# Kernel tuning notes

Hardware: AMD Instinct MI355X
Metric: run time of the kernel (lower is better)

## Reference

```python
import jax, jax.numpy as jnp
import numpy as np

B, S, D, H = 2, 2048, 1024, 16
DK = D // H


def setup_inputs() -> dict:
    key = jax.random.key(0)
    ks = jax.random.split(key, 14)
    inp = {
        'query': jax.random.normal(ks[0], (B, S, D), jnp.float32),
        'key': jax.random.normal(ks[1], (B, S, D), jnp.float32),
        'value': jax.random.normal(ks[2], (B, S, D), jnp.float32),
        'mask': jax.random.randint(ks[3], (B, 1, S, S), 0, 2).astype(bool),
        'rel_pos_bias': jax.random.normal(ks[4], (1, H, S, S), jnp.float32),
    }
    scale = 1.0 / np.sqrt(D)
    names = ['Wq', 'bq', 'Wk', 'bk', 'Wv', 'bv', 'Wo', 'bo']
    for i, n in enumerate(names):
        k = ks[5 + i]
        if n.startswith('W'):
            inp[n] = jax.random.normal(k, (D, D), jnp.float32) * scale
        else:
            inp[n] = jnp.zeros((D,), jnp.float32)
    return inp


def reference(query, key, value, mask, rel_pos_bias, Wq, bq, Wk, bk, Wv, bv, Wo, bo):
    # torch Linear: y = x @ W^T + b; W stored [out, in]
    def proj(x, W, b):
        y = x @ W.T + b                       # [B,S,D]
        return y.reshape(B, S, H, DK).transpose(0, 2, 1, 3)  # [B,H,S,DK]

    q = proj(query, Wq, bq)
    k = proj(key, Wk, bk)
    v = proj(value, Wv, bv)

    scores = jnp.einsum('bhqd,bhkd->bhqk', q, k) / jnp.sqrt(jnp.float32(DK))
    scores = scores + rel_pos_bias
    scores = jnp.where(mask, jnp.float32(-1e9), scores)
    p_attn = jax.nn.softmax(scores, axis=-1)
    x = jnp.einsum('bhqk,bhkd->bhqd', p_attn, v)  # [B,H,S,DK]
    x = x.transpose(0, 2, 1, 3).reshape(B, S, D)
    return x @ Wo.T + bo
```

## Files before the change

### kernel.cpp

```cpp
#include <hip/hip_runtime.h>
#include <stdint.h>


typedef _Float16 f16;
typedef _Float16 f16x8 __attribute__((ext_vector_type(8)));
typedef _Float16 f16x4 __attribute__((ext_vector_type(4)));
typedef float f32x4 __attribute__((ext_vector_type(4)));

#define LOG2E 1.44269504088896340736f

__device__ __forceinline__ void gload16(const void* g, void* l) {
  __builtin_amdgcn_global_load_lds(
      (const __attribute__((address_space(1))) unsigned int*)g,
      (__attribute__((address_space(3))) unsigned int*)l, 16, 0, 0);
}

struct CvtSrcs { const float* s[7]; };

__global__ __launch_bounds__(256) void cvt_all(CvtSrcs a, f16* __restrict__ out) {
  const int i = blockIdx.x * 256 + threadIdx.x;
  int r, base;
  if (i < 3145728) { r = i >> 20; base = r << 20; }
  else { r = 3 + ((i - 3145728) >> 18); base = 3145728 + ((r - 3) << 18); }
  const float4 v = ((const float4*)a.s[r])[i - base];
  f16x4 o = {(f16)v.x, (f16)v.y, (f16)v.z, (f16)v.w};
  ((f16x4*)out)[i] = o;
}

__global__ void mask_detect(const uint8_t* __restrict__ m, int* __restrict__ flag) {
  __shared__ int s_off, s_weird;
  const int t = threadIdx.x;
  if (t == 0) { s_off = 0; s_weird = 0; }
  __syncthreads();
  int f_off = 0, f_weird = 0;
  for (int i = t; i < 8192; i += 256) {
    const uint8_t v = m[i];
    if ((i & 3) && v) f_off = 1;
    if (v > 1) f_weird = 1;
  }
  if (f_off) atomicOr(&s_off, 1);
  if (f_weird) atomicOr(&s_weird, 1);
  __syncthreads();
  if (t == 0) *flag = (s_off && !s_weird) ? 1 : 0;
}

__global__ __launch_bounds__(256) void mask_canon(const uint8_t* __restrict__ m,
                                                  uint8_t* __restrict__ out,
                                                  const int* __restrict__ flag) {
  const int i = (blockIdx.x * 256 + threadIdx.x) * 4;
  uchar4 o;
  if (*flag) {
    const uchar4 v = *(const uchar4*)(m + i);
    o = make_uchar4(v.x != 0, v.y != 0, v.z != 0, v.w != 0);
  } else {
    const int4 v = *(const int4*)((const int*)m + i);
    o = make_uchar4(v.x != 0, v.y != 0, v.z != 0, v.w != 0);
  }
  *(uchar4*)(out + i) = o;
}

__global__ __launch_bounds__(256, 2) void gemm_qkv(
    const f16* __restrict__ qh, const f16* __restrict__ kh, const f16* __restrict__ vh,
    const f16* __restrict__ wq, const f16* __restrict__ wk, const f16* __restrict__ wv,
    const float* __restrict__ bq, const float* __restrict__ bk, const float* __restrict__ bv,
    f16* __restrict__ Qp, f16* __restrict__ Kp, f16* __restrict__ Vt) {
  constexpr int K = 1024;
  const int t = threadIdx.x;
  const int w = t >> 6, lane = t & 63, l15 = lane & 15, l4 = lane >> 4;
  const int nt = (int)blockIdx.x % 48;
  const int bm = ((int)blockIdx.x / 48) * 128;
  const int which = nt >> 4;
  const int bn = (nt & 15) * 64;
  const f16* A = which == 0 ? qh : which == 1 ? kh : vh;
  const f16* Bw = which == 0 ? wq : which == 1 ? wk : wv;
  const float* bias = which == 0 ? bq : which == 1 ? bk : bv;

  __shared__ f16 As[2][128 * 32];
  __shared__ f16 Bs[2][64 * 32];

  const f16* a0 = A + (size_t)(bm + (t >> 2)) * K + (t & 3) * 8;
  const f16* a1 = a0 + (size_t)64 * K;
  const f16* b0 = Bw + (size_t)(bn + (t >> 2)) * K + (t & 3) * 8;

  f32x4 acc[2][4];
#pragma unroll
  for (int m = 0; m < 2; ++m)
#pragma unroll
    for (int n = 0; n < 4; ++n) acc[m][n] = (f32x4){0.f, 0.f, 0.f, 0.f};

#define STAGE_G(buf, k0)                          \
  do {                                            \
    gload16(a0 + (k0), &As[buf][w * 512]);        \
    gload16(a1 + (k0), &As[buf][2048 + w * 512]); \
    gload16(b0 + (k0), &Bs[buf][w * 512]);        \
  } while (0)

  STAGE_G(0, 0);
  __syncthreads();
  int cur = 0;
#pragma unroll 1
  for (int kt = 0; kt < 32; ++kt) {
    if (kt < 31) STAGE_G(cur ^ 1, (kt + 1) * 32);
    const f16* ap = &As[cur][(w * 32 + l15) * 32 + l4 * 8];
    const f16* bp = &Bs[cur][l15 * 32 + l4 * 8];
    f16x8 af[2], bfr[4];
#pragma unroll
    for (int m = 0; m < 2; ++m) af[m] = *(const f16x8*)(ap + m * 512);
#pragma unroll
    for (int n = 0; n < 4; ++n) bfr[n] = *(const f16x8*)(bp + n * 512);
#pragma unroll
    for (int m = 0; m < 2; ++m)
#pragma unroll
      for (int n = 0; n < 4; ++n)
        acc[m][n] = __builtin_amdgcn_mfma_f32_16x16x32_f16(af[m], bfr[n], acc[m][n], 0, 0, 0);
    __syncthreads();
    cur ^= 1;
  }
#undef STAGE_G

  const float scale = which == 0 ? 0.125f * LOG2E : 1.0f;
  f16* outp = which == 0 ? Qp : which == 1 ? Kp : Vt;
#pragma unroll
  for (int m = 0; m < 2; ++m) {
    const int r0 = bm + w * 32 + m * 16 + (l4 << 2);
#pragma unroll
    for (int n = 0; n < 4; ++n) {
      const int c = bn + n * 16 + l15;
      const float bv = bias[c];
#pragma unroll
      for (int j = 0; j < 4; ++j) {
        const int r = r0 + j;
        const float v = (acc[m][n][j] + bv) * scale;
        const int b_ = r >> 11, s = r & 2047, h_ = c >> 6, dk = c & 63;
        if (which < 2)
          outp[(((size_t)b_ * 16 + h_) * 2048 + s) * 64 + dk] = (f16)v;
        else
          outp[(((size_t)b_ * 16 + h_) * 64 + dk) * 2048 + s] = (f16)v;
      }
    }
  }
}

__global__ __launch_bounds__(256, 2) void gemm_out(const f16* __restrict__ A,
                                                   const f16* __restrict__ Bw,
                                                   const float* __restrict__ bias,
                                                   float* __restrict__ outp) {
  constexpr int K = 1024;
  const int t = threadIdx.x;
  const int w = t >> 6, lane = t & 63, l15 = lane & 15, l4 = lane >> 4;
  const int bm = (int)(blockIdx.x >> 4) * 128;
  const int bn = (int)(blockIdx.x & 15) * 64;

  __shared__ f16 As[2][128 * 32];
  __shared__ f16 Bs[2][64 * 32];

  const f16* a0 = A + (size_t)(bm + (t >> 2)) * K + (t & 3) * 8;
  const f16* a1 = a0 + (size_t)64 * K;
  const f16* b0 = Bw + (size_t)(bn + (t >> 2)) * K + (t & 3) * 8;

  f32x4 acc[2][4];
#pragma unroll
  for (int m = 0; m < 2; ++m)
#pragma unroll
    for (int n = 0; n < 4; ++n) acc[m][n] = (f32x4){0.f, 0.f, 0.f, 0.f};

#define STAGE_G(buf, k0)                          \
  do {                                            \
    gload16(a0 + (k0), &As[buf][w * 512]);        \
    gload16(a1 + (k0), &As[buf][2048 + w * 512]); \
    gload16(b0 + (k0), &Bs[buf][w * 512]);        \
  } while (0)

  STAGE_G(0, 0);
  __syncthreads();
  int cur = 0;
#pragma unroll 1
  for (int kt = 0; kt < 32; ++kt) {
    if (kt < 31) STAGE_G(cur ^ 1, (kt + 1) * 32);
    const f16* ap = &As[cur][(w * 32 + l15) * 32 + l4 * 8];
    const f16* bp = &Bs[cur][l15 * 32 + l4 * 8];
    f16x8 af[2], bfr[4];
#pragma unroll
    for (int m = 0; m < 2; ++m) af[m] = *(const f16x8*)(ap + m * 512);
#pragma unroll
    for (int n = 0; n < 4; ++n) bfr[n] = *(const f16x8*)(bp + n * 512);
#pragma unroll
    for (int m = 0; m < 2; ++m)
#pragma unroll
      for (int n = 0; n < 4; ++n)
        acc[m][n] = __builtin_amdgcn_mfma_f32_16x16x32_f16(af[m], bfr[n], acc[m][n], 0, 0, 0);
    __syncthreads();
    cur ^= 1;
  }
#undef STAGE_G

#pragma unroll
  for (int m = 0; m < 2; ++m) {
    const int r0 = bm + w * 32 + m * 16 + (l4 << 2);
#pragma unroll
    for (int n = 0; n < 4; ++n) {
      const int c = bn + n * 16 + l15;
      const float bv = bias[c];
#pragma unroll
      for (int j = 0; j < 4; ++j)
        outp[(size_t)(r0 + j) * 1024 + c] = acc[m][n][j] + bv;
    }
  }
}

__device__ __forceinline__ const f16x8* swzr(const f16* base, int row, int bytecol) {
  return (const f16x8*)((const char*)base + row * 128 + (bytecol ^ ((row & 7) << 4)));
}

__global__ __launch_bounds__(256, 4) void attn_fwd(
    const f16* __restrict__ Qp, const f16* __restrict__ Kp,
    const f16* __restrict__ Vt, const float* __restrict__ bias,
    const uint8_t* __restrict__ mask, f16* __restrict__ X) {
  constexpr int S = 2048;
  const int bid = blockIdx.x;
  const int qt = bid & 31, b = (bid >> 5) & 1, h = bid >> 6;
  const int t = threadIdx.x, w = t >> 6, lane = t & 63;
  const int l15 = lane & 15, l4 = lane >> 4;
  const int q0 = qt * 64 + w * 16;

  const f16* Qbh = Qp + (size_t)(b * 16 + h) * S * 64;
  const f16* Kbh = Kp + (size_t)(b * 16 + h) * S * 64;
  const f16* Vbh = Vt + (size_t)(b * 16 + h) * 64 * S;
  const float* biasr = bias + (size_t)h * S * S + (size_t)(q0 + l15) * S + l4 * 4;
  const uint8_t* maskr = mask + (size_t)b * S * S + (size_t)(q0 + l15) * S + l4 * 4;

  __shared__ f16 Ks[2][64 * 64];
  __shared__ f16 Vs[2][64 * 64];
  __shared__ f16 Ps[4][16 * 64];

  f16x8 qf[2];
#pragma unroll
  for (int ks = 0; ks < 2; ++ks)
    qf[ks] = *(const f16x8*)(Qbh + (size_t)(q0 + l15) * 64 + ks * 32 + l4 * 8);

  f32x4 oacc[4];
#pragma unroll
  for (int n = 0; n < 4; ++n) oacc[n] = (f32x4){0.f, 0.f, 0.f, 0.f};
  float mrow = -3e38f, lrow = 0.f;

  const int srow = t >> 3;
  const int scol = (((t & 7) ^ (srow & 7)) << 3);

#define STAGE(bf, kk)                                                               \
  do {                                                                              \
    gload16(Kbh + (size_t)((kk) + srow) * 64 + scol, &Ks[bf][w * 512]);             \
    gload16(Kbh + (size_t)((kk) + 32 + srow) * 64 + scol, &Ks[bf][2048 + w * 512]); \
    gload16(Vbh + (size_t)srow * S + (kk) + scol, &Vs[bf][w * 512]);                \
    gload16(Vbh + (size_t)(32 + srow) * S + (kk) + scol, &Vs[bf][2048 + w * 512]);  \
  } while (0)

  STAGE(0, 0);
  STAGE(1, 64);

#pragma unroll 1
  for (int kt = 0; kt < 32; ++kt) {
    const int k0 = kt * 64;
    const int buf = kt & 1;
    asm volatile("s_waitcnt vmcnt(4)" ::: "memory");
    __builtin_amdgcn_s_barrier();

    f32x4 bc[4];
    uint32_t mc[4];
#pragma unroll
    for (int n = 0; n < 4; ++n) {
      bc[n] = *(const f32x4*)(biasr + k0 + n * 16);
      mc[n] = *(const uint32_t*)(maskr + k0 + n * 16);
    }

    f32x4 sacc[4];
#pragma unroll
    for (int n = 0; n < 4; ++n) sacc[n] = (f32x4){0.f, 0.f, 0.f, 0.f};
#pragma unroll
    for (int n = 0; n < 4; ++n)
#pragma unroll
      for (int ks = 0; ks < 2; ++ks) {
        const f16x8 kf = *swzr(&Ks[buf][0], n * 16 + l15, ks * 64 + l4 * 16);
        sacc[n] = __builtin_amdgcn_mfma_f32_16x16x32_f16(kf, qf[ks], sacc[n], 0, 0, 0);
      }

    float tmax = -3e38f;
#pragma unroll
    for (int n = 0; n < 4; ++n)
#pragma unroll
      for (int j = 0; j < 4; ++j) {
        float s = fmaf(bc[n][j], LOG2E, sacc[n][j]);
        s = ((mc[n] >> (8 * j)) & 255u) ? -1.44269504e9f : s;
        sacc[n][j] = s;
        tmax = fmaxf(tmax, s);
      }
    tmax = fmaxf(tmax, __shfl_xor(tmax, 16));
    tmax = fmaxf(tmax, __shfl_xor(tmax, 32));

    const float mnew = fmaxf(mrow, tmax);
    const float alpha = __builtin_exp2f(mrow - mnew);
    mrow = mnew;
    float lsum = 0.f;
#pragma unroll
    for (int n = 0; n < 4; ++n)
#pragma unroll
      for (int j = 0; j < 4; ++j) {
        const float e = __builtin_exp2f(sacc[n][j] - mnew);
        sacc[n][j] = e;
        lsum += e;
      }
    lsum += __shfl_xor(lsum, 16);
    lsum += __shfl_xor(lsum, 32);
    lrow = lrow * alpha + lsum;

    float aq[4];
#pragma unroll
    for (int j = 0; j < 4; ++j) aq[j] = __shfl(alpha, l4 * 4 + j);
#pragma unroll
    for (int n = 0; n < 4; ++n)
#pragma unroll
      for (int j = 0; j < 4; ++j) oacc[n][j] *= aq[j];

#pragma unroll
    for (int n = 0; n < 4; ++n) {
      f16x4 pk = {(f16)sacc[n][0], (f16)sacc[n][1], (f16)sacc[n][2], (f16)sacc[n][3]};
      *(f16x4*)((char*)&Ps[w][0] + l15 * 128 +
                ((32 * n + 8 * l4) ^ ((l15 & 7) << 4))) = pk;
    }

    f16x8 pf[2];
#pragma unroll
    for (int ks = 0; ks < 2; ++ks) pf[ks] = *swzr(&Ps[w][0], l15, ks * 64 + l4 * 16);
#pragma unroll
    for (int ks = 0; ks < 2; ++ks)
#pragma unroll
      for (int n = 0; n < 4; ++n) {
        const f16x8 vf = *swzr(&Vs[buf][0], n * 16 + l15, ks * 64 + l4 * 16);
        oacc[n] = __builtin_amdgcn_mfma_f32_16x16x32_f16(pf[ks], vf, oacc[n], 0, 0, 0);
      }

    __builtin_amdgcn_s_barrier();
    STAGE(buf, (k0 + 128) & (S - 1));
  }
#undef STAGE

  asm volatile("s_waitcnt vmcnt(0)" ::: "memory");

  const float inv = 1.0f / lrow;
  float invq[4];
#pragma unroll
  for (int j = 0; j < 4; ++j) invq[j] = __shfl(inv, l4 * 4 + j);
#pragma unroll
  for (int j = 0; j < 4; ++j) {
    const int qrow = q0 + l4 * 4 + j;
#pragma unroll
    for (int n = 0; n < 4; ++n)
      X[((size_t)b * 2048 + qrow) * 1024 + h * 64 + n * 16 + l15] =
          (f16)(oacc[n][j] * invq[j]);
  }
}

extern "C" void kernel_launch(void* const* d_in, const int* in_sizes, int n_in,
                              void* d_out, int out_size, void* d_ws, size_t ws_size,
                              hipStream_t stream) {
  const float* query = (const float*)d_in[0];
  const float* key_ = (const float*)d_in[1];
  const float* value = (const float*)d_in[2];
  const uint8_t* mask = (const uint8_t*)d_in[3];
  const float* bias = (const float*)d_in[4];
  const float* Wq = (const float*)d_in[5];
  const float* bq = (const float*)d_in[6];
  const float* Wk = (const float*)d_in[7];
  const float* bk = (const float*)d_in[8];
  const float* Wv = (const float*)d_in[9];
  const float* bv = (const float*)d_in[10];
  const float* Wo = (const float*)d_in[11];
  const float* bo = (const float*)d_in[12];

  char* p = (char*)d_ws;
  f16* qh = (f16*)p; p += (size_t)4194304 * 2;
  f16* kh = (f16*)p; p += (size_t)4194304 * 2;
  f16* vh = (f16*)p; p += (size_t)4194304 * 2;
  f16* wqh = (f16*)p; p += (size_t)1048576 * 2;
  f16* wkh = (f16*)p; p += (size_t)1048576 * 2;
  f16* wvh = (f16*)p; p += (size_t)1048576 * 2;
  f16* woh = (f16*)p; p += (size_t)1048576 * 2;
  f16* Qp = (f16*)p; p += (size_t)4194304 * 2;
  f16* Kp = (f16*)p; p += (size_t)4194304 * 2;
  f16* Vt = (f16*)p; p += (size_t)4194304 * 2;
  f16* Xh = (f16*)p; p += (size_t)4194304 * 2;
  uint8_t* m8 = (uint8_t*)p; p += (size_t)8388608;
  int* flag = (int*)p; p += 256;
  if (ws_size < (size_t)(p - (char*)d_ws)) return;

  mask_detect<<<1, 256, 0, stream>>>(mask, flag);
  mask_canon<<<8192, 256, 0, stream>>>(mask, m8, flag);

  CvtSrcs cs;
  cs.s[0] = query; cs.s[1] = key_; cs.s[2] = value;
  cs.s[3] = Wq; cs.s[4] = Wk; cs.s[5] = Wv; cs.s[6] = Wo;
  cvt_all<<<16384, 256, 0, stream>>>(cs, qh);

  gemm_qkv<<<1536, 256, 0, stream>>>(qh, kh, vh, wqh, wkh, wvh, bq, bk, bv,
                                     Qp, Kp, Vt);

  attn_fwd<<<1024, 256, 0, stream>>>(Qp, Kp, Vt, bias, m8, Xh);

  gemm_out<<<512, 256, 0, stream>>>(Xh, woh, bo, (float*)d_out);
}
```

Baseline: 288.5 us.

## Process both batches per attention block to reuse relative position bias loads

Each attention block now handles the same head and query tile for both batch elements, so every bias tile read from global memory serves two softmax computations. This halves the traffic on the large fp32 bias tensor. The grid is halved, launch bounds drop to 2 waves per SIMD, and the K/V double buffering is replaced by single-buffered per-batch tiles with full syncthreads, which exposes load latency. The masked select becomes an fma with the mask value, and the P conversion uses packed round-toward-zero converts.

```diff
diff --git a/kernel.cpp b/kernel.cpp
--- a/kernel.cpp
+++ b/kernel.cpp
@@ -5,6 +5,7 @@
 typedef _Float16 f16;
 typedef _Float16 f16x8 __attribute__((ext_vector_type(8)));
 typedef _Float16 f16x4 __attribute__((ext_vector_type(4)));
+typedef __fp16 h2 __attribute__((ext_vector_type(2)));
 typedef float f32x4 __attribute__((ext_vector_type(4)));
 
 #define LOG2E 1.44269504088896340736f
@@ -212,150 +213,173 @@
   return (const f16x8*)((const char*)base + row * 128 + (bytecol ^ ((row & 7) << 4)));
 }
 
-__global__ __launch_bounds__(256, 4) void attn_fwd(
+__global__ __launch_bounds__(256, 2) void attn_fwd(
     const f16* __restrict__ Qp, const f16* __restrict__ Kp,
     const f16* __restrict__ Vt, const float* __restrict__ bias,
     const uint8_t* __restrict__ mask, f16* __restrict__ X) {
   constexpr int S = 2048;
   const int bid = blockIdx.x;
-  const int qt = bid & 31, b = (bid >> 5) & 1, h = bid >> 6;
+  const int qt = bid & 31, h = bid >> 5;
   const int t = threadIdx.x, w = t >> 6, lane = t & 63;
   const int l15 = lane & 15, l4 = lane >> 4;
   const int q0 = qt * 64 + w * 16;
 
-  const f16* Qbh = Qp + (size_t)(b * 16 + h) * S * 64;
-  const f16* Kbh = Kp + (size_t)(b * 16 + h) * S * 64;
-  const f16* Vbh = Vt + (size_t)(b * 16 + h) * 64 * S;
+  const f16* Qb[2] = {Qp + (size_t)h * S * 64, Qp + (size_t)(16 + h) * S * 64};
+  const f16* Kb[2] = {Kp + (size_t)h * S * 64, Kp + (size_t)(16 + h) * S * 64};
+  const f16* Vb[2] = {Vt + (size_t)h * 64 * S, Vt + (size_t)(16 + h) * 64 * S};
   const float* biasr = bias + (size_t)h * S * S + (size_t)(q0 + l15) * S + l4 * 4;
-  const uint8_t* maskr = mask + (size_t)b * S * S + (size_t)(q0 + l15) * S + l4 * 4;
+  const uint8_t* mr0 = mask + (size_t)(q0 + l15) * S + l4 * 4;
+  const uint8_t* mr1 = mr0 + (size_t)S * S;
 
   __shared__ f16 Ks[2][64 * 64];
   __shared__ f16 Vs[2][64 * 64];
   __shared__ f16 Ps[4][16 * 64];
 
-  f16x8 qf[2];
-#pragma unroll
-  for (int ks = 0; ks < 2; ++ks)
-    qf[ks] = *(const f16x8*)(Qbh + (size_t)(q0 + l15) * 64 + ks * 32 + l4 * 8);
-
-  f32x4 oacc[4];
-#pragma unroll
-  for (int n = 0; n < 4; ++n) oacc[n] = (f32x4){0.f, 0.f, 0.f, 0.f};
-  float mrow = -3e38f, lrow = 0.f;
+  f16x8 qf[2][2];
+#pragma unroll
+  for (int bb = 0; bb < 2; ++bb)
+#pragma unroll
+    for (int ks = 0; ks < 2; ++ks)
+      qf[bb][ks] =
+          *(const f16x8*)(Qb[bb] + (size_t)(q0 + l15) * 64 + ks * 32 + l4 * 8);
+
+  f32x4 oacc[2][4];
+#pragma unroll
+  for (int bb = 0; bb < 2; ++bb)
+#pragma unroll
+    for (int n = 0; n < 4; ++n) oacc[bb][n] = (f32x4){0.f, 0.f, 0.f, 0.f};
+  float mrow[2] = {-3e38f, -3e38f}, lrow[2] = {0.f, 0.f};
 
   const int srow = t >> 3;
   const int scol = (((t & 7) ^ (srow & 7)) << 3);
 
-#define STAGE(bf, kk)                                                               \
+#define STAGE(kk)                                                                   \
   do {                                                                              \
-    gload16(Kbh + (size_t)((kk) + srow) * 64 + scol, &Ks[bf][w * 512]);             \
-    gload16(Kbh + (size_t)((kk) + 32 + srow) * 64 + scol, &Ks[bf][2048 + w * 512]); \
-    gload16(Vbh + (size_t)srow * S + (kk) + scol, &Vs[bf][w * 512]);                \
-    gload16(Vbh + (size_t)(32 + srow) * S + (kk) + scol, &Vs[bf][2048 + w * 512]);  \
+    gload16(Kb[0] + (size_t)((kk) + srow) * 64 + scol, &Ks[0][w * 512]);            \
+    gload16(Kb[0] + (size_t)((kk) + 32 + srow) * 64 + scol, &Ks[0][2048 + w * 512]);\
+    gload16(Kb[1] + (size_t)((kk) + srow) * 64 + scol, &Ks[1][w * 512]);            \
+    gload16(Kb[1] + (size_t)((kk) + 32 + srow) * 64 + scol, &Ks[1][2048 + w * 512]);\
+    gload16(Vb[0] + (size_t)srow * S + (kk) + scol, &Vs[0][w * 512]);               \
+    gload16(Vb[0] + (size_t)(32 + srow) * S + (kk) + scol, &Vs[0][2048 + w * 512]); \
+    gload16(Vb[1] + (size_t)srow * S + (kk) + scol, &Vs[1][w * 512]);               \
+    gload16(Vb[1] + (size_t)(32 + srow) * S + (kk) + scol, &Vs[1][2048 + w * 512]); \
   } while (0)
 
-  STAGE(0, 0);
-  STAGE(1, 64);
+  STAGE(0);
 
 #pragma unroll 1
   for (int kt = 0; kt < 32; ++kt) {
     const int k0 = kt * 64;
-    const int buf = kt & 1;
-    asm volatile("s_waitcnt vmcnt(4)" ::: "memory");
-    __builtin_amdgcn_s_barrier();
-
     f32x4 bc[4];
-    uint32_t mc[4];
+    uint32_t mc[2][4];
 #pragma unroll
     for (int n = 0; n < 4; ++n) {
       bc[n] = *(const f32x4*)(biasr + k0 + n * 16);
-      mc[n] = *(const uint32_t*)(maskr + k0 + n * 16);
+      mc[0][n] = *(const uint32_t*)(mr0 + k0 + n * 16);
+      mc[1][n] = *(const uint32_t*)(mr1 + k0 + n * 16);
     }
-
-    f32x4 sacc[4];
-#pragma unroll
-    for (int n = 0; n < 4; ++n) sacc[n] = (f32x4){0.f, 0.f, 0.f, 0.f};
-#pragma unroll
-    for (int n = 0; n < 4; ++n)
-#pragma unroll
-      for (int ks = 0; ks < 2; ++ks) {
-        const f16x8 kf = *swzr(&Ks[buf][0], n * 16 + l15, ks * 64 + l4 * 16);
-        sacc[n] = __builtin_amdgcn_mfma_f32_16x16x32_f16(kf, qf[ks], sacc[n], 0, 0, 0);
+    __syncthreads();
+
+    f32x4 sacc[2][4];
+#pragma unroll
+    for (int bb = 0; bb < 2; ++bb)
+#pragma unroll
+      for (int n = 0; n < 4; ++n) sacc[bb][n] = (f32x4){0.f, 0.f, 0.f, 0.f};
+#pragma unroll
+    for (int bb = 0; bb < 2; ++bb)
+#pragma unroll
+      for (int n = 0; n < 4; ++n)
+#pragma unroll
+        for (int ks = 0; ks < 2; ++ks) {
+          const f16x8 kf = *swzr(&Ks[bb][0], n * 16 + l15, ks * 64 + l4 * 16);
+          sacc[bb][n] =
+              __builtin_amdgcn_mfma_f32_16x16x32_f16(kf, qf[bb][ks], sacc[bb][n], 0, 0, 0);
+        }
+
+#pragma unroll
+    for (int bb = 0; bb < 2; ++bb) {
+      float tmax = -3e38f;
+#pragma unroll
+      for (int n = 0; n < 4; ++n) {
+#pragma unroll
+        for (int j = 0; j < 4; ++j) {
+          const float mf = (float)((mc[bb][n] >> (8 * j)) & 255u);
+          sacc[bb][n][j] = fmaf(mf, -2e9f, fmaf(bc[n][j], LOG2E, sacc[bb][n][j]));
+        }
+        tmax = fmaxf(tmax, fmaxf(fmaxf(sacc[bb][n][0], sacc[bb][n][1]),
+                                 fmaxf(sacc[bb][n][2], sacc[bb][n][3])));
       }
-
-    float tmax = -3e38f;
-#pragma unroll
-    for (int n = 0; n < 4; ++n)
-#pragma unroll
-      for (int j = 0; j < 4; ++j) {
-        float s = fmaf(bc[n][j], LOG2E, sacc[n][j]);
-        s = ((mc[n] >> (8 * j)) & 255u) ? -1.44269504e9f : s;
-        sacc[n][j] = s;
-        tmax = fmaxf(tmax, s);
+      tmax = fmaxf(tmax, __shfl_xor(tmax, 16));
+      tmax = fmaxf(tmax, __shfl_xor(tmax, 32));
+
+      const float mnew = fmaxf(mrow[bb], tmax);
+      const float alpha = __builtin_exp2f(mrow[bb] - mnew);
+      mrow[bb] = mnew;
+      float lsum = 0.f;
+#pragma unroll
+      for (int n = 0; n < 4; ++n)
+#pragma unroll
+        for (int j = 0; j < 4; ++j) {
+          const float e = __builtin_exp2f(sacc[bb][n][j] - mnew);
+          sacc[bb][n][j] = e;
+          lsum += e;
+        }
+      lsum += __shfl_xor(lsum, 16);
+      lsum += __shfl_xor(lsum, 32);
+      lrow[bb] = lrow[bb] * alpha + lsum;
+
+      float aq[4];
+#pragma unroll
+      for (int j = 0; j < 4; ++j) aq[j] = __shfl(alpha, l4 * 4 + j);
+#pragma unroll
+      for (int n = 0; n < 4; ++n)
+#pragma unroll
+        for (int j = 0; j < 4; ++j) oacc[bb][n][j] *= aq[j];
+
+#pragma unroll
+      for (int n = 0; n < 4; ++n) {
+        h2 p01 = __builtin_amdgcn_cvt_pkrtz(sacc[bb][n][0], sacc[bb][n][1]);
+        h2 p23 = __builtin_amdgcn_cvt_pkrtz(sacc[bb][n][2], sacc[bb][n][3]);
+        f16x4 pk;
+        pk[0] = (f16)p01[0]; pk[1] = (f16)p01[1];
+        pk[2] = (f16)p23[0]; pk[3] = (f16)p23[1];
+        *(f16x4*)((char*)&Ps[w][0] + l15 * 128 +
+                  ((32 * n + 8 * l4) ^ ((l15 & 7) << 4))) = pk;
       }
-    tmax = fmaxf(tmax, __shfl_xor(tmax, 16));
-    tmax = fmaxf(tmax, __shfl_xor(tmax, 32));
-
-    const float mnew = fmaxf(mrow, tmax);
-    const float alpha = __builtin_exp2f(mrow - mnew);
-    mrow = mnew;
-    float lsum = 0.f;
-#pragma unroll
-    for (int n = 0; n < 4; ++n)
-#pragma unroll
-      for (int j = 0; j < 4; ++j) {
-        const float e = __builtin_exp2f(sacc[n][j] - mnew);
-        sacc[n][j] = e;
-        lsum += e;
-      }
-    lsum += __shfl_xor(lsum, 16);
-    lsum += __shfl_xor(lsum, 32);
-    lrow = lrow * alpha + lsum;
-
-    float aq[4];
-#pragma unroll
-    for (int j = 0; j < 4; ++j) aq[j] = __shfl(alpha, l4 * 4 + j);
-#pragma unroll
-    for (int n = 0; n < 4; ++n)
-#pragma unroll
-      for (int j = 0; j < 4; ++j) oacc[n][j] *= aq[j];
-
-#pragma unroll
-    for (int n = 0; n < 4; ++n) {
-      f16x4 pk = {(f16)sacc[n][0], (f16)sacc[n][1], (f16)sacc[n][2], (f16)sacc[n][3]};
-      *(f16x4*)((char*)&Ps[w][0] + l15 * 128 +
-                ((32 * n + 8 * l4) ^ ((l15 & 7) << 4))) = pk;
+
+      f16x8 pf[2];
+#pragma unroll
+      for (int ks = 0; ks < 2; ++ks)
+        pf[ks] = *swzr(&Ps[w][0], l15, ks * 64 + l4 * 16);
+#pragma unroll
+      for (int ks = 0; ks < 2; ++ks)
+#pragma unroll
+        for (int n = 0; n < 4; ++n) {
+          const f16x8 vf = *swzr(&Vs[bb][0], n * 16 + l15, ks * 64 + l4 * 16);
+          oacc[bb][n] =
+              __builtin_amdgcn_mfma_f32_16x16x32_f16(pf[ks], vf, oacc[bb][n], 0, 0, 0);
+        }
     }
 
-    f16x8 pf[2];
-#pragma unroll
-    for (int ks = 0; ks < 2; ++ks) pf[ks] = *swzr(&Ps[w][0], l15, ks * 64 + l4 * 16);
-#pragma unroll
-    for (int ks = 0; ks < 2; ++ks)
-#pragma unroll
-      for (int n = 0; n < 4; ++n) {
-        const f16x8 vf = *swzr(&Vs[buf][0], n * 16 + l15, ks * 64 + l4 * 16);
-        oacc[n] = __builtin_amdgcn_mfma_f32_16x16x32_f16(pf[ks], vf, oacc[n], 0, 0, 0);
-      }
-
-    __builtin_amdgcn_s_barrier();
-    STAGE(buf, (k0 + 128) & (S - 1));
+    __syncthreads();
+    if (kt < 31) STAGE(k0 + 64);
   }
 #undef STAGE
 
-  asm volatile("s_waitcnt vmcnt(0)" ::: "memory");
-
-  const float inv = 1.0f / lrow;
-  float invq[4];
-#pragma unroll
-  for (int j = 0; j < 4; ++j) invq[j] = __shfl(inv, l4 * 4 + j);
-#pragma unroll
-  for (int j = 0; j < 4; ++j) {
-    const int qrow = q0 + l4 * 4 + j;
-#pragma unroll
-    for (int n = 0; n < 4; ++n)
-      X[((size_t)b * 2048 + qrow) * 1024 + h * 64 + n * 16 + l15] =
-          (f16)(oacc[n][j] * invq[j]);
+#pragma unroll
+  for (int bb = 0; bb < 2; ++bb) {
+    const float inv = 1.0f / lrow[bb];
+    float invq[4];
+#pragma unroll
+    for (int j = 0; j < 4; ++j) invq[j] = __shfl(inv, l4 * 4 + j);
+#pragma unroll
+    for (int j = 0; j < 4; ++j) {
+      const int qrow = q0 + l4 * 4 + j;
+#pragma unroll
+      for (int n = 0; n < 4; ++n)
+        X[((size_t)bb * 2048 + qrow) * 1024 + h * 64 + n * 16 + l15] =
+            (f16)(oacc[bb][n][j] * invq[j]);
+    }
   }
 }
 
@@ -403,7 +427,7 @@
   gemm_qkv<<<1536, 256, 0, stream>>>(qh, kh, vh, wqh, wkh, wvh, bq, bk, bv,
                                      Qp, Kp, Vt);
 
-  attn_fwd<<<1024, 256, 0, stream>>>(Qp, Kp, Vt, bias, m8, Xh);
+  attn_fwd<<<512, 256, 0, stream>>>(Qp, Kp, Vt, bias, m8, Xh);
 
   gemm_out<<<512, 256, 0, stream>>>(Xh, woh, bo, (float*)d_out);
 }
```

New measurement: 256.6 us. 1.12x faster.
